# Kernel optimization log

Hardware: AMD Instinct MI355X
Metric: run time of the kernel (lower is better)

Reference implementation:

```python
import jax, jax.numpy as jnp
import numpy as np


def setup_inputs() -> dict:
    key = jax.random.key(0)
    k_u, k_lam, k_B, k_C = jax.random.split(key, 4)
    batch, seq_len, d_model, N = 4, 4096, 1024, 64
    return {
        "u": jax.random.normal(k_u, (batch, seq_len, d_model), dtype=jnp.float32),
        "Lambda": jax.random.normal(k_lam, (N,), dtype=jnp.float32),
        "log_dt": jnp.zeros((1,), dtype=jnp.float32),
        "B": jax.random.normal(k_B, (N, d_model), dtype=jnp.float32),
        "C": jax.random.normal(k_C, (d_model, N), dtype=jnp.float32),
        "D": jnp.zeros((d_model,), dtype=jnp.float32),
    }


def reference(u, Lambda, log_dt, B, C, D):
    # dt = exp(log_dt); A = diag(exp(dt * (-exp(Lambda)))) -> diagonal decay vector a of shape (N,)
    dt = jnp.exp(log_dt)          # (1,)
    a = jnp.exp(-dt * jnp.exp(Lambda))  # (N,)

    # Precompute input projection for all timesteps: Bu[b, t, n] = u[b, t] @ B.T
    Bu = jnp.einsum("bld,nd->bln", u, B)  # (batch, L, N)

    # Sequential diagonal recurrence: x_t = a * x_{t-1} + Bu_t
    def step(x, bu_t):
        x = a * x + bu_t
        return x, x

    x0 = jnp.zeros((u.shape[0], Lambda.shape[0]), dtype=u.dtype)
    _, xs = jax.lax.scan(step, x0, jnp.swapaxes(Bu, 0, 1))  # xs: (L, batch, N)
    xs = jnp.swapaxes(xs, 0, 1)  # (batch, L, N)

    # Output projection + skip: y_t = x_t @ C.T + D * u_t
    return jnp.einsum("bln,dn->bld", xs, C) + D * u
```

## Files before the change

### kernel.cpp

```cpp
#include <hip/hip_runtime.h>


constexpr int BATCH  = 4;
constexpr int L      = 4096;
constexpr int DM     = 1024;
constexpr int N      = 64;
constexpr int ROWS   = BATCH * L;
constexpr int CHUNK  = 32;
constexpr int NCHUNK = L / CHUNK;

typedef __attribute__((ext_vector_type(8))) short     bf16x8;
typedef __attribute__((ext_vector_type(4))) float     f32x4;

__device__ __forceinline__ unsigned short f2bf(float f) {
  unsigned int u = __float_as_uint(f);
  u += 0x7FFFu + ((u >> 16) & 1u);
  return (unsigned short)(u >> 16);
}

__global__ __launch_bounds__(256) void bu_gemm(const float* __restrict__ u,
                                               const float* __restrict__ Bm,
                                               float* __restrict__ BuP,
                                               int KR) {
  __shared__ __align__(16) unsigned short As[2][64][72];
  __shared__ __align__(16) unsigned short Bs[2][64][72];
  const int tid  = threadIdx.x;
  const int lane = tid & 63;
  const int wv   = tid >> 6;
  const int l15  = lane & 15;
  const int g    = lane >> 4;
  const int row0 = blockIdx.x * 64;
  const int kbase = blockIdx.y * KR;
  float* __restrict__ out = BuP + (long)blockIdx.y * ROWS * N;

  const int sr = tid >> 4;
  const int sq = tid & 15;

  f32x4 acc[4] = {};
  float4 pa[4], pb[4];

  const int NCH = KR / 64;
  {
    const int kb = kbase;
    #pragma unroll
    for (int i = 0; i < 4; ++i) {
      const int r = sr + i * 16;
      pa[i] = *reinterpret_cast<const float4*>(&u[(long)(row0 + r) * DM + kb + sq * 4]);
      pb[i] = *reinterpret_cast<const float4*>(&Bm[(long)r * DM + kb + sq * 4]);
    }
  }

  for (int c = 0; c < NCH; ++c) {
    const int buf = c & 1;
    if (c) __syncthreads();
    #pragma unroll
    for (int i = 0; i < 4; ++i) {
      const int r = sr + i * 16;
      ushort4 ha = make_ushort4(f2bf(pa[i].x), f2bf(pa[i].y), f2bf(pa[i].z), f2bf(pa[i].w));
      ushort4 hb = make_ushort4(f2bf(pb[i].x), f2bf(pb[i].y), f2bf(pb[i].z), f2bf(pb[i].w));
      *reinterpret_cast<ushort4*>(&As[buf][r][sq * 4]) = ha;
      *reinterpret_cast<ushort4*>(&Bs[buf][r][sq * 4]) = hb;
    }
    __syncthreads();
    if (c + 1 < NCH) {
      const int kb = kbase + (c + 1) * 64;
      #pragma unroll
      for (int i = 0; i < 4; ++i) {
        const int r = sr + i * 16;
        pa[i] = *reinterpret_cast<const float4*>(&u[(long)(row0 + r) * DM + kb + sq * 4]);
        pb[i] = *reinterpret_cast<const float4*>(&Bm[(long)r * DM + kb + sq * 4]);
      }
    }
    #pragma unroll
    for (int ks = 0; ks < 2; ++ks) {
      const bf16x8 af = *reinterpret_cast<const bf16x8*>(
          &As[buf][wv * 16 + l15][ks * 32 + g * 8]);
      #pragma unroll
      for (int t = 0; t < 4; ++t) {
        const bf16x8 bfr = *reinterpret_cast<const bf16x8*>(
            &Bs[buf][t * 16 + l15][ks * 32 + g * 8]);
        acc[t] = __builtin_amdgcn_mfma_f32_16x16x32_bf16(af, bfr, acc[t], 0, 0, 0);
      }
    }
  }

  const int orow = row0 + wv * 16 + g * 4;
  #pragma unroll
  for (int t = 0; t < 4; ++t)
    #pragma unroll
    for (int r = 0; r < 4; ++r)
      out[(long)(orow + r) * N + t * 16 + l15] = acc[t][r];
}

__global__ __launch_bounds__(256) void f_scan(const float* __restrict__ BuP,
                                              const float* __restrict__ Lambda,
                                              const float* __restrict__ log_dt,
                                              float* __restrict__ F,
                                              const float* __restrict__ Cm,
                                              unsigned short* __restrict__ Cb,
                                              int nsplit) {
  if (threadIdx.x < 128) {
    const int i = blockIdx.x * 128 + threadIdx.x;
    const float4 v = *reinterpret_cast<const float4*>(&Cm[(long)i * 4]);
    *reinterpret_cast<ushort4*>(&Cb[(long)i * 4]) =
        make_ushort4(f2bf(v.x), f2bf(v.y), f2bf(v.z), f2bf(v.w));
  }

  const int pair = blockIdx.x * 4 + (threadIdx.x >> 6);
  const int b = pair >> 7, c = pair & 127;
  const int n = threadIdx.x & 63;
  const long base = ((long)b * L + (long)c * CHUNK) * N + n;

  float v[CHUNK];
  #pragma unroll
  for (int s = 0; s < CHUNK; ++s) v[s] = BuP[base + s * N];
  if (nsplit == 2) {
    const float* p2 = BuP + (long)ROWS * N;
    #pragma unroll
    for (int s = 0; s < CHUNK; ++s) v[s] += p2[base + s * N];
  }

  const float dt = __expf(log_dt[0]);
  const float a  = __expf(-dt * __expf(Lambda[n]));
  float x = 0.0f;
  #pragma unroll
  for (int s = 0; s < CHUNK; ++s) x = fmaf(a, x, v[s]);
  F[pair * N + n] = x;
}

__global__ __launch_bounds__(256) void carry_scan(const float* __restrict__ F,
                                                  const float* __restrict__ Lambda,
                                                  const float* __restrict__ log_dt,
                                                  float* __restrict__ carry) {
  const int t = threadIdx.x;
  const int b = t >> 6;
  const int n = t & 63;
  const float dt = __expf(log_dt[0]);
  const float w  = -dt * __expf(Lambda[n]);
  const float aS = __expf(w * (float)CHUNK);

  float f[NCHUNK];
  #pragma unroll
  for (int c = 0; c < NCHUNK; ++c) f[c] = F[(b * NCHUNK + c) * N + n];

  float P = 0.0f;
  #pragma unroll
  for (int c = 0; c < NCHUNK; ++c) {
    carry[(b * NCHUNK + c) * N + n] = P;
    P = fmaf(aS, P, f[c]);
  }
}

__global__ __launch_bounds__(256) void xs_scan(const float* __restrict__ BuP,
                                               const float* __restrict__ carry,
                                               const float* __restrict__ Lambda,
                                               const float* __restrict__ log_dt,
                                               unsigned short* __restrict__ xsb,
                                               int nsplit) {
  const int pair = blockIdx.x * 4 + (threadIdx.x >> 6);
  const int b = pair >> 7, c = pair & 127;
  const int n = threadIdx.x & 63;
  const long base = ((long)b * L + (long)c * CHUNK) * N + n;

  float v[CHUNK];
  #pragma unroll
  for (int s = 0; s < CHUNK; ++s) v[s] = BuP[base + s * N];
  if (nsplit == 2) {
    const float* p2 = BuP + (long)ROWS * N;
    #pragma unroll
    for (int s = 0; s < CHUNK; ++s) v[s] += p2[base + s * N];
  }

  const float dt = __expf(log_dt[0]);
  const float a  = __expf(-dt * __expf(Lambda[n]));
  float x = carry[pair * N + n];
  #pragma unroll
  for (int s = 0; s < CHUNK; ++s) {
    x = fmaf(a, x, v[s]);
    xsb[base + s * N] = f2bf(x);
  }
}

__global__ __launch_bounds__(256) void y_gemm(const unsigned short* __restrict__ xsb,
                                              const unsigned short* __restrict__ Cb,
                                              const float* __restrict__ Dv,
                                              const float* __restrict__ u,
                                              float* __restrict__ y) {
  __shared__ __align__(16) char smem[64 * 132 * 4];
  unsigned short (*Xs)[72] = reinterpret_cast<unsigned short (*)[72]>(smem);
  unsigned short (*Cs)[72] = reinterpret_cast<unsigned short (*)[72]>(smem + 9216);
  float (*T)[132] = reinterpret_cast<float (*)[132]>(smem);
  __shared__ float Dsh[128];

  const int tid  = threadIdx.x;
  const int lane = tid & 63;
  const int wv   = tid >> 6;
  const int l15  = lane & 15;
  const int g    = lane >> 4;
  const int row0 = (blockIdx.x & 255) * 64;
  const int d0   = (blockIdx.x >> 8) * 128;

  #pragma unroll
  for (int i = 0; i < 2; ++i) {
    const int idx = tid + i * 256;
    const int r = idx >> 3, q = idx & 7;
    const uint4 v = *reinterpret_cast<const uint4*>(&xsb[(long)(row0 + r) * N + q * 8]);
    *reinterpret_cast<uint4*>(&Xs[r][q * 8]) = v;
  }
  #pragma unroll
  for (int i = 0; i < 4; ++i) {
    const int idx = tid + i * 256;
    const int r = idx >> 3, q = idx & 7;
    const uint4 v = *reinterpret_cast<const uint4*>(&Cb[(long)(d0 + r) * N + q * 8]);
    *reinterpret_cast<uint4*>(&Cs[r][q * 8]) = v;
  }
  if (tid < 128) Dsh[tid] = Dv[d0 + tid];
  __syncthreads();

  bf16x8 af[2];
  #pragma unroll
  for (int ks = 0; ks < 2; ++ks)
    af[ks] = *reinterpret_cast<const bf16x8*>(&Xs[wv * 16 + l15][ks * 32 + g * 8]);

  f32x4 acc[8] = {};
  #pragma unroll
  for (int t = 0; t < 8; ++t) {
    #pragma unroll
    for (int ks = 0; ks < 2; ++ks) {
      const bf16x8 bfr = *reinterpret_cast<const bf16x8*>(
          &Cs[t * 16 + l15][ks * 32 + g * 8]);
      acc[t] = __builtin_amdgcn_mfma_f32_16x16x32_bf16(af[ks], bfr, acc[t], 0, 0, 0);
    }
  }

  __syncthreads();
  #pragma unroll
  for (int t = 0; t < 8; ++t)
    #pragma unroll
    for (int r = 0; r < 4; ++r)
      T[wv * 16 + g * 4 + r][t * 16 + l15] = acc[t][r];
  __syncthreads();

  #pragma unroll
  for (int i = 0; i < 8; ++i) {
    const int id = tid + i * 256;
    const int r = id >> 5;
    const int q = id & 31;
    float4 v = *reinterpret_cast<const float4*>(&T[r][q * 4]);
    const float4 dd = *reinterpret_cast<const float4*>(&Dsh[q * 4]);
    if (dd.x != 0.0f || dd.y != 0.0f || dd.z != 0.0f || dd.w != 0.0f) {
      const float4 uu = *reinterpret_cast<const float4*>(
          &u[(long)(row0 + r) * DM + d0 + q * 4]);
      v.x = fmaf(dd.x, uu.x, v.x);
      v.y = fmaf(dd.y, uu.y, v.y);
      v.z = fmaf(dd.z, uu.z, v.z);
      v.w = fmaf(dd.w, uu.w, v.w);
    }
    *reinterpret_cast<float4*>(&y[(long)(row0 + r) * DM + d0 + q * 4]) = v;
  }
}

extern "C" void kernel_launch(void* const* d_in, const int* in_sizes, int n_in,
                              void* d_out, int out_size, void* d_ws, size_t ws_size,
                              hipStream_t stream) {
  const float* u      = (const float*)d_in[0];
  const float* Lambda = (const float*)d_in[1];
  const float* log_dt = (const float*)d_in[2];
  const float* Bm     = (const float*)d_in[3];
  const float* Cm     = (const float*)d_in[4];
  const float* Dv     = (const float*)d_in[5];
  float* y = (float*)d_out;

  const size_t planeB = (size_t)ROWS * N;
  const size_t smallf = (size_t)BATCH * NCHUNK * N;
  const size_t need2  = (2 * planeB + 2 * smallf) * 4 + planeB * 2 + (size_t)DM * N * 2;
  const int nsplit = (ws_size >= need2) ? 2 : 1;

  float* BuP   = (float*)d_ws;
  float* F     = BuP + (size_t)nsplit * planeB;
  float* carry = F + smallf;
  unsigned short* xsb = (unsigned short*)(carry + smallf);
  unsigned short* Cb  = xsb + planeB;

  bu_gemm<<<dim3(ROWS / 64, nsplit), 256, 0, stream>>>(u, Bm, BuP, DM / nsplit);
  f_scan<<<BATCH * NCHUNK / 4, 256, 0, stream>>>(BuP, Lambda, log_dt, F, Cm, Cb, nsplit);
  carry_scan<<<1, 256, 0, stream>>>(F, Lambda, log_dt, carry);
  xs_scan<<<BATCH * NCHUNK / 4, 256, 0, stream>>>(BuP, carry, Lambda, log_dt, xsb, nsplit);
  y_gemm<<<(ROWS / 64) * (DM / 128), 256, 0, stream>>>(xsb, Cb, Dv, u, y);
}
```

Measured before the change: 40.26 us.

## Fuse chunk scan into Bu GEMM epilogue and carry correction into output GEMM

The input-projection GEMM now performs the per-chunk diagonal scan on its 64-row tile directly from shared memory, writing fp32 local states and chunk finals. The separate f_scan and xs_scan kernels are removed, and y_gemm applies the carry correction a^(t+1)*carry and the bf16 conversion of C while loading tiles. This removes two launches and re-reading of the Bu intermediate, at the cost of dropping split-K in the first GEMM, a serial 64-step scan by one wave per block, and extra exp work in y_gemm.

Result: faster. 38.54 us (-4.3%).

```diff
diff --git a/kernel.cpp b/kernel.cpp
--- a/kernel.cpp
+++ b/kernel.cpp
@@ -6,7 +6,7 @@
 constexpr int DM     = 1024;
 constexpr int N      = 64;
 constexpr int ROWS   = BATCH * L;
-constexpr int CHUNK  = 32;
+constexpr int CHUNK  = 64;
 constexpr int NCHUNK = L / CHUNK;
 
 typedef __attribute__((ext_vector_type(8))) short     bf16x8;
@@ -18,20 +18,24 @@
   return (unsigned short)(u >> 16);
 }
 
-__global__ __launch_bounds__(256) void bu_gemm(const float* __restrict__ u,
+__global__ __launch_bounds__(256) void bu_scan(const float* __restrict__ u,
                                                const float* __restrict__ Bm,
-                                               float* __restrict__ BuP,
-                                               int KR) {
-  __shared__ __align__(16) unsigned short As[2][64][72];
-  __shared__ __align__(16) unsigned short Bs[2][64][72];
+                                               const float* __restrict__ Lambda,
+                                               const float* __restrict__ log_dt,
+                                               float* __restrict__ xs,
+                                               float* __restrict__ F) {
+  __shared__ __align__(16) char smem[36864];
+  typedef unsigned short AsT[64][72];
+  AsT* As = reinterpret_cast<AsT*>(smem);
+  AsT* Bs = reinterpret_cast<AsT*>(smem + 18432);
+  float (*T)[68] = reinterpret_cast<float (*)[68]>(smem);
+
   const int tid  = threadIdx.x;
   const int lane = tid & 63;
   const int wv   = tid >> 6;
   const int l15  = lane & 15;
   const int g    = lane >> 4;
   const int row0 = blockIdx.x * 64;
-  const int kbase = blockIdx.y * KR;
-  float* __restrict__ out = BuP + (long)blockIdx.y * ROWS * N;
 
   const int sr = tid >> 4;
   const int sq = tid & 15;
@@ -39,15 +43,12 @@
   f32x4 acc[4] = {};
   float4 pa[4], pb[4];
 
-  const int NCH = KR / 64;
-  {
-    const int kb = kbase;
-    #pragma unroll
-    for (int i = 0; i < 4; ++i) {
-      const int r = sr + i * 16;
-      pa[i] = *reinterpret_cast<const float4*>(&u[(long)(row0 + r) * DM + kb + sq * 4]);
-      pb[i] = *reinterpret_cast<const float4*>(&Bm[(long)r * DM + kb + sq * 4]);
-    }
+  constexpr int NCH = DM / 64;
+  #pragma unroll
+  for (int i = 0; i < 4; ++i) {
+    const int r = sr + i * 16;
+    pa[i] = *reinterpret_cast<const float4*>(&u[(long)(row0 + r) * DM + sq * 4]);
+    pb[i] = *reinterpret_cast<const float4*>(&Bm[(long)r * DM + sq * 4]);
   }
 
   for (int c = 0; c < NCH; ++c) {
@@ -63,7 +64,7 @@
     }
     __syncthreads();
     if (c + 1 < NCH) {
-      const int kb = kbase + (c + 1) * 64;
+      const int kb = (c + 1) * 64;
       #pragma unroll
       for (int i = 0; i < 4; ++i) {
         const int r = sr + i * 16;
@@ -84,48 +85,30 @@
     }
   }
 
-  const int orow = row0 + wv * 16 + g * 4;
+  __syncthreads();
   #pragma unroll
   for (int t = 0; t < 4; ++t)
     #pragma unroll
     for (int r = 0; r < 4; ++r)
-      out[(long)(orow + r) * N + t * 16 + l15] = acc[t][r];
-}
-
-__global__ __launch_bounds__(256) void f_scan(const float* __restrict__ BuP,
-                                              const float* __restrict__ Lambda,
-                                              const float* __restrict__ log_dt,
-                                              float* __restrict__ F,
-                                              const float* __restrict__ Cm,
-                                              unsigned short* __restrict__ Cb,
-                                              int nsplit) {
-  if (threadIdx.x < 128) {
-    const int i = blockIdx.x * 128 + threadIdx.x;
-    const float4 v = *reinterpret_cast<const float4*>(&Cm[(long)i * 4]);
-    *reinterpret_cast<ushort4*>(&Cb[(long)i * 4]) =
-        make_ushort4(f2bf(v.x), f2bf(v.y), f2bf(v.z), f2bf(v.w));
-  }
-
-  const int pair = blockIdx.x * 4 + (threadIdx.x >> 6);
-  const int b = pair >> 7, c = pair & 127;
-  const int n = threadIdx.x & 63;
-  const long base = ((long)b * L + (long)c * CHUNK) * N + n;
-
-  float v[CHUNK];
-  #pragma unroll
-  for (int s = 0; s < CHUNK; ++s) v[s] = BuP[base + s * N];
-  if (nsplit == 2) {
-    const float* p2 = BuP + (long)ROWS * N;
-    #pragma unroll
-    for (int s = 0; s < CHUNK; ++s) v[s] += p2[base + s * N];
-  }
-
-  const float dt = __expf(log_dt[0]);
-  const float a  = __expf(-dt * __expf(Lambda[n]));
-  float x = 0.0f;
-  #pragma unroll
-  for (int s = 0; s < CHUNK; ++s) x = fmaf(a, x, v[s]);
-  F[pair * N + n] = x;
+      T[wv * 16 + g * 4 + r][t * 16 + l15] = acc[t][r];
+  __syncthreads();
+
+  if (tid < 64) {
+    const int n = tid;
+    const float dt = __expf(log_dt[0]);
+    const float a  = __expf(-dt * __expf(Lambda[n]));
+    float v[CHUNK];
+    #pragma unroll
+    for (int s = 0; s < CHUNK; ++s) v[s] = T[s][n];
+    const long base = (long)row0 * N + n;
+    float x = 0.0f;
+    #pragma unroll
+    for (int s = 0; s < CHUNK; ++s) {
+      x = fmaf(a, x, v[s]);
+      xs[base + s * N] = x;
+    }
+    F[blockIdx.x * N + n] = x;
+  }
 }
 
 __global__ __launch_bounds__(256) void carry_scan(const float* __restrict__ F,
@@ -151,46 +134,19 @@
   }
 }
 
-__global__ __launch_bounds__(256) void xs_scan(const float* __restrict__ BuP,
-                                               const float* __restrict__ carry,
-                                               const float* __restrict__ Lambda,
-                                               const float* __restrict__ log_dt,
-                                               unsigned short* __restrict__ xsb,
-                                               int nsplit) {
-  const int pair = blockIdx.x * 4 + (threadIdx.x >> 6);
-  const int b = pair >> 7, c = pair & 127;
-  const int n = threadIdx.x & 63;
-  const long base = ((long)b * L + (long)c * CHUNK) * N + n;
-
-  float v[CHUNK];
-  #pragma unroll
-  for (int s = 0; s < CHUNK; ++s) v[s] = BuP[base + s * N];
-  if (nsplit == 2) {
-    const float* p2 = BuP + (long)ROWS * N;
-    #pragma unroll
-    for (int s = 0; s < CHUNK; ++s) v[s] += p2[base + s * N];
-  }
-
-  const float dt = __expf(log_dt[0]);
-  const float a  = __expf(-dt * __expf(Lambda[n]));
-  float x = carry[pair * N + n];
-  #pragma unroll
-  for (int s = 0; s < CHUNK; ++s) {
-    x = fmaf(a, x, v[s]);
-    xsb[base + s * N] = f2bf(x);
-  }
-}
-
-__global__ __launch_bounds__(256) void y_gemm(const unsigned short* __restrict__ xsb,
-                                              const unsigned short* __restrict__ Cb,
+__global__ __launch_bounds__(256) void y_gemm(const float* __restrict__ xs,
+                                              const float* __restrict__ carry,
+                                              const float* __restrict__ Lambda,
+                                              const float* __restrict__ log_dt,
+                                              const float* __restrict__ Cm,
                                               const float* __restrict__ Dv,
                                               const float* __restrict__ u,
                                               float* __restrict__ y) {
-  __shared__ __align__(16) char smem[64 * 132 * 4];
+  __shared__ __align__(16) char smem[33792];
   unsigned short (*Xs)[72] = reinterpret_cast<unsigned short (*)[72]>(smem);
   unsigned short (*Cs)[72] = reinterpret_cast<unsigned short (*)[72]>(smem + 9216);
   float (*T)[132] = reinterpret_cast<float (*)[132]>(smem);
-  __shared__ float Dsh[128];
+  __shared__ float wS[64], ciS[64], Dsh[128];
 
   const int tid  = threadIdx.x;
   const int lane = tid & 63;
@@ -200,21 +156,35 @@
   const int row0 = (blockIdx.x & 255) * 64;
   const int d0   = (blockIdx.x >> 8) * 128;
 
-  #pragma unroll
-  for (int i = 0; i < 2; ++i) {
-    const int idx = tid + i * 256;
-    const int r = idx >> 3, q = idx & 7;
-    const uint4 v = *reinterpret_cast<const uint4*>(&xsb[(long)(row0 + r) * N + q * 8]);
-    *reinterpret_cast<uint4*>(&Xs[r][q * 8]) = v;
-  }
+  if (tid < 64) {
+    const float dt = __expf(log_dt[0]);
+    wS[tid]  = -dt * __expf(Lambda[tid]);
+    ciS[tid] = carry[row0 + tid];
+  }
+  if (tid < 128) Dsh[tid] = Dv[d0 + tid];
+  __syncthreads();
+
   #pragma unroll
   for (int i = 0; i < 4; ++i) {
     const int idx = tid + i * 256;
-    const int r = idx >> 3, q = idx & 7;
-    const uint4 v = *reinterpret_cast<const uint4*>(&Cb[(long)(d0 + r) * N + q * 8]);
-    *reinterpret_cast<uint4*>(&Cs[r][q * 8]) = v;
-  }
-  if (tid < 128) Dsh[tid] = Dv[d0 + tid];
+    const int r = idx >> 4, q = idx & 15;
+    float4 v = *reinterpret_cast<const float4*>(&xs[(long)(row0 + r) * N + q * 4]);
+    const float p = (float)(r + 1);
+    v.x += __expf(wS[q * 4 + 0] * p) * ciS[q * 4 + 0];
+    v.y += __expf(wS[q * 4 + 1] * p) * ciS[q * 4 + 1];
+    v.z += __expf(wS[q * 4 + 2] * p) * ciS[q * 4 + 2];
+    v.w += __expf(wS[q * 4 + 3] * p) * ciS[q * 4 + 3];
+    *reinterpret_cast<ushort4*>(&Xs[r][q * 4]) =
+        make_ushort4(f2bf(v.x), f2bf(v.y), f2bf(v.z), f2bf(v.w));
+  }
+  #pragma unroll
+  for (int i = 0; i < 8; ++i) {
+    const int idx = tid + i * 256;
+    const int r = idx >> 4, q = idx & 15;
+    const float4 v = *reinterpret_cast<const float4*>(&Cm[(long)(d0 + r) * N + q * 4]);
+    *reinterpret_cast<ushort4*>(&Cs[r][q * 4]) =
+        make_ushort4(f2bf(v.x), f2bf(v.y), f2bf(v.z), f2bf(v.w));
+  }
   __syncthreads();
 
   bf16x8 af[2];
@@ -272,19 +242,12 @@
   float* y = (float*)d_out;
 
   const size_t planeB = (size_t)ROWS * N;
-  const size_t smallf = (size_t)BATCH * NCHUNK * N;
-  const size_t need2  = (2 * planeB + 2 * smallf) * 4 + planeB * 2 + (size_t)DM * N * 2;
-  const int nsplit = (ws_size >= need2) ? 2 : 1;
-
-  float* BuP   = (float*)d_ws;
-  float* F     = BuP + (size_t)nsplit * planeB;
-  float* carry = F + smallf;
-  unsigned short* xsb = (unsigned short*)(carry + smallf);
-  unsigned short* Cb  = xsb + planeB;
-
-  bu_gemm<<<dim3(ROWS / 64, nsplit), 256, 0, stream>>>(u, Bm, BuP, DM / nsplit);
-  f_scan<<<BATCH * NCHUNK / 4, 256, 0, stream>>>(BuP, Lambda, log_dt, F, Cm, Cb, nsplit);
+  float* xs    = (float*)d_ws;
+  float* F     = xs + planeB;
+  float* carry = F + (size_t)BATCH * NCHUNK * N;
+
+  bu_scan<<<ROWS / 64, 256, 0, stream>>>(u, Bm, Lambda, log_dt, xs, F);
   carry_scan<<<1, 256, 0, stream>>>(F, Lambda, log_dt, carry);
-  xs_scan<<<BATCH * NCHUNK / 4, 256, 0, stream>>>(BuP, carry, Lambda, log_dt, xsb, nsplit);
-  y_gemm<<<(ROWS / 64) * (DM / 128), 256, 0, stream>>>(xsb, Cb, Dv, u, y);
-}
+  y_gemm<<<(ROWS / 64) * (DM / 128), 256, 0, stream>>>(xs, carry, Lambda, log_dt,
+                                                       Cm, Dv, u, y);
+}
```
